# Kernel optimization log

Hardware: AMD Instinct MI355X
Metric: run time of the kernel (lower is better)

## Reference

```python
import jax, jax.numpy as jnp
import numpy as np

N = 50000      # nodes
E = 800000     # edges (before self-loops)
IN, HID, HEADS, OUT = 128, 16, 8, 64
NEG_SLOPE = 0.2
EPS = 1e-16


def gat_layer(x, edge_index, W, att_src, att_dst, bias, heads, ch, num_nodes, concat):
    # x: [N, F_in]; edge_index: [2, E'] (row0 = source j, row1 = target i)
    h = (x @ W).reshape(-1, heads, ch)                     # [N, H, C]
    a_src = jnp.sum(h * att_src, axis=-1)                  # [N, H]
    a_dst = jnp.sum(h * att_dst, axis=-1)                  # [N, H]
    src, dst = edge_index[0], edge_index[1]
    alpha = a_src[src] + a_dst[dst]                        # [E', H]
    alpha = jax.nn.leaky_relu(alpha, NEG_SLOPE)
    # segment softmax over incoming edges of each target node
    m = jax.ops.segment_max(alpha, dst, num_segments=num_nodes)
    alpha = jnp.exp(alpha - m[dst])
    denom = jax.ops.segment_sum(alpha, dst, num_segments=num_nodes)
    alpha = alpha / (denom[dst] + EPS)
    msg = h[src] * alpha[:, :, None]                       # [E', H, C]
    out = jax.ops.segment_sum(msg, dst, num_segments=num_nodes)  # [N, H, C]
    out = out.reshape(-1, heads * ch) if concat else out.mean(axis=1)
    return out + bias


def gat_model(x, edge_index, W1, att_src1, att_dst1, b1, W2, att_src2, att_dst2, b2, num_nodes):
    # PyG GATConv default add_self_loops=True
    loops = jnp.arange(num_nodes, dtype=edge_index.dtype)
    ei = jnp.concatenate([edge_index, jnp.stack([loops, loops])], axis=1)
    h = gat_layer(x, ei, W1, att_src1, att_dst1, b1, HEADS, HID, num_nodes, concat=True)
    h = jax.nn.relu(h)
    return gat_layer(h, ei, W2, att_src2, att_dst2, b2, 1, OUT, num_nodes, concat=False)


def setup_inputs() -> dict:
    key = jax.random.key(0)
    ks = jax.random.split(key, 10)
    x = jax.random.normal(ks[0], (N, IN), jnp.float32)
    edge_index = jax.random.randint(ks[1], (2, E), 0, N, dtype=jnp.int32)
    W1 = jax.random.normal(ks[2], (IN, HEADS * HID), jnp.float32) / np.sqrt(IN).astype(np.float32)
    att_src1 = jax.random.normal(ks[3], (HEADS, HID), jnp.float32) * 0.1
    att_dst1 = jax.random.normal(ks[4], (HEADS, HID), jnp.float32) * 0.1
    b1 = jnp.zeros((HEADS * HID,), jnp.float32)
    W2 = jax.random.normal(ks[5], (HEADS * HID, OUT), jnp.float32) / np.sqrt(HEADS * HID).astype(np.float32)
    att_src2 = jax.random.normal(ks[6], (1, OUT), jnp.float32) * 0.1
    att_dst2 = jax.random.normal(ks[7], (1, OUT), jnp.float32) * 0.1
    b2 = jnp.zeros((OUT,), jnp.float32)
    return {"x": x, "edge_index": edge_index, "W1": W1, "att_src1": att_src1,
            "att_dst1": att_dst1, "b1": b1, "W2": W2, "att_src2": att_src2,
            "att_dst2": att_dst2, "b2": b2, "num_nodes": N}


def reference(x, edge_index, W1, att_src1, att_dst1, b1, W2, att_src2, att_dst2, b2, num_nodes):
    return gat_model(x, edge_index, W1, att_src1, att_dst1, b1,
                     W2, att_src2, att_dst2, b2, num_nodes)
```

## Files before the change

kernel.cpp:

```cpp
#include <hip/hip_runtime.h>

#define NEG 0.2f
#define EPSV 1e-16f
#define EPB 4096
#define CAPN 64
#define CAPB (256 * 18)

typedef _Float16 h4 __attribute__((ext_vector_type(4)));
typedef _Float16 h8 __attribute__((ext_vector_type(8)));
typedef float f32x4 __attribute__((ext_vector_type(4)));

__device__ __forceinline__ float lrelu(float x) { return x > 0.f ? x : NEG * x; }

__global__ void k_setup(const float* __restrict__ W1, _Float16* __restrict__ Wt1,
                        const float* __restrict__ W2, _Float16* __restrict__ Wt2,
                        int* __restrict__ bcur, int nbuckets) {
  const int bid = blockIdx.x, tid = threadIdx.x;
  if (bid < 64) {
    int t = bid * 256 + tid;
    int c = t >> 7, k = t & 127;
    Wt1[t] = (_Float16)W1[k * 128 + c];
  } else if (bid < 96) {
    int t = (bid - 64) * 256 + tid;
    if (t < 64 * 128) {
      int c = t >> 7, k = t & 127;
      Wt2[t] = (_Float16)W2[k * 64 + c];
    }
  } else {
    if (tid < nbuckets) bcur[tid] = tid * CAPB;
  }
}

__global__ __launch_bounds__(256) void k_bin_gemm1(
    const int* __restrict__ src, const int* __restrict__ dst, int* __restrict__ bcur,
    unsigned* __restrict__ binned, int E, int nBinB, const float* __restrict__ X,
    const _Float16* __restrict__ Wt, const float* __restrict__ atts,
    const float* __restrict__ attd, _Float16* __restrict__ Hout,
    float* __restrict__ as_, float* __restrict__ ad_, int N) {
  constexpr int K = 128, XS = 136;
  __shared__ _Float16 xs[64 * XS];
  const int tid = threadIdx.x;

  if ((int)blockIdx.x < nBinB) {
    int* hist = (int*)xs;
    int* base = hist + 256;
    const int b0 = blockIdx.x * EPB;
    const int b1 = min(b0 + EPB, E);
    hist[tid] = 0;
    __syncthreads();
    for (int e = b0 + tid; e < b1; e += 256) atomicAdd(&hist[dst[e] >> 8], 1);
    __syncthreads();
    int h = hist[tid];
    if (h > 0) base[tid] = atomicAdd(&bcur[tid], h);
    __syncthreads();
    hist[tid] = 0;
    __syncthreads();
    for (int e = b0 + tid; e < b1; e += 256) {
      int d = dst[e];
      int bk = d >> 8;
      int pos = base[bk] + atomicAdd(&hist[bk], 1);
      binned[pos] = ((unsigned)(d & 255) << 16) | (unsigned)src[e];
    }
    return;
  }

  const int bid = blockIdx.x - nBinB;
  const int wv = tid >> 6, lane = tid & 63;
  const long row0 = (long)bid * 64;
  const int nrow = (int)min((long)64, (long)N - row0);

  for (int idx = tid; idx < 64 * (K / 4); idx += 256) {
    int r = idx >> 5, iw = idx & 31;
    float4 v = make_float4(0.f, 0.f, 0.f, 0.f);
    if (r < nrow) v = *(const float4*)&X[(row0 + r) * K + iw * 4];
    h4 o;
    o[0] = (_Float16)v.x;
    o[1] = (_Float16)v.y;
    o[2] = (_Float16)v.z;
    o[3] = (_Float16)v.w;
    *(h4*)&xs[r * XS + iw * 4] = o;
  }
  __syncthreads();

  const int rlo = lane & 15, khi = lane >> 4;
  h8 a[4];
#pragma unroll
  for (int kb = 0; kb < 4; kb++)
    a[kb] = *(const h8*)&xs[(wv * 16 + rlo) * XS + kb * 32 + khi * 8];
  __syncthreads();

  const int orow = wv * 16 + khi * 4;
#pragma unroll
  for (int n = 0; n < 8; n++) {
    f32x4 acc = {0.f, 0.f, 0.f, 0.f};
#pragma unroll
    for (int kb = 0; kb < 4; kb++) {
      h8 b = *(const h8*)&Wt[(n * 16 + rlo) * K + kb * 32 + khi * 8];
      acc = __builtin_amdgcn_mfma_f32_16x16x32_f16(a[kb], b, acc, 0, 0, 0);
    }
#pragma unroll
    for (int r = 0; r < 4; r++) {
      _Float16 hv = (_Float16)acc[r];
      xs[(orow + r) * XS + n * 16 + rlo] = hv;
      if (orow + r < nrow) Hout[(row0 + orow + r) * 128 + n * 16 + rlo] = hv;
    }
  }
  __syncthreads();
  for (int t = tid; t < 64 * 8; t += 256) {
    int r = t >> 3, h = t & 7;
    if (r < nrow) {
      const _Float16* hp = &xs[r * XS + h * 16];
      const float* sp = &atts[h * 16];
      const float* dp = &attd[h * 16];
      float s = 0.f, d = 0.f;
#pragma unroll
      for (int c = 0; c < 16; c++) {
        float v = (float)hp[c];
        s += v * sp[c];
        d += v * dp[c];
      }
      as_[(row0 + r) * 8 + h] = s;
      ad_[(row0 + r) * 8 + h] = d;
    }
  }
}

__global__ __launch_bounds__(256) void k_unbin(const unsigned* __restrict__ binned,
                                               const int* __restrict__ bcur,
                                               unsigned short* __restrict__ csr_src,
                                               int* __restrict__ deg, int N) {
  __shared__ int cnt[256];
  const int n0 = blockIdx.x << 8;
  const int start = blockIdx.x * CAPB;
  const int end = bcur[blockIdx.x];
  cnt[threadIdx.x] = 0;
  __syncthreads();
  for (int t = start + (int)threadIdx.x; t < end; t += 256) {
    unsigned v = binned[t];
    int dl = (int)(v >> 16);
    int pos = atomicAdd(&cnt[dl], 1);
    if (pos < CAPN) csr_src[(long)(n0 + dl) * CAPN + pos] = (unsigned short)(v & 0xFFFFu);
  }
  __syncthreads();
  int n = n0 + (int)threadIdx.x;
  if (n < N) deg[n] = min(cnt[threadIdx.x], CAPN);
}

__global__ __launch_bounds__(256) void k_n1g2(
    const int* __restrict__ deg_, const unsigned short* __restrict__ csr_src,
    const _Float16* __restrict__ Hf, const float* __restrict__ as1,
    const float* __restrict__ ad1, const float* __restrict__ b1,
    const _Float16* __restrict__ Wt2, const float* __restrict__ s2,
    const float* __restrict__ dd2, _Float16* __restrict__ H2,
    float* __restrict__ as2, float* __restrict__ ad2, int N) {
  constexpr int K = 128, XS = 136;
  __shared__ _Float16 xs[64 * XS];
  const int tid = threadIdx.x;
  const int wv = tid >> 6, lane = tid & 63;
  const long row0 = (long)blockIdx.x * 64;
  const int nrow = (int)min((long)64, (long)N - row0);
  const int sub = lane >> 4, ln = lane & 15;
  const int f0 = ln * 8, hf = ln >> 1;

  for (int t = 0; t < 16; t++) {
    const int r = wv * 16 + t;
    const long i = row0 + r;
    if (i < N) {
      const int deg = deg_[i];
      const long beg = i * CAPN;
      const float adh = ad1[i * 8 + hf];
      const float pself = __expf(lrelu(as1[i * 8 + hf] + adh));
      float acc[8] = {0.f, 0.f, 0.f, 0.f, 0.f, 0.f, 0.f, 0.f};
      float sp = 0.f;
      int e = sub;
      for (; e + 4 < deg; e += 8) {
        int j0 = (int)csr_src[beg + e], j1 = (int)csr_src[beg + e + 4];
        float p0 = __expf(lrelu(as1[j0 * 8 + hf] + adh));
        float p1 = __expf(lrelu(as1[j1 * 8 + hf] + adh));
        h8 v0 = *(const h8*)&Hf[(long)j0 * 128 + f0];
        h8 v1 = *(const h8*)&Hf[(long)j1 * 128 + f0];
        sp += p0 + p1;
#pragma unroll
        for (int c = 0; c < 8; c++) acc[c] += p0 * (float)v0[c] + p1 * (float)v1[c];
      }
      for (; e < deg; e += 4) {
        int j = (int)csr_src[beg + e];
        float p = __expf(lrelu(as1[j * 8 + hf] + adh));
        h8 v = *(const h8*)&Hf[(long)j * 128 + f0];
        sp += p;
#pragma unroll
        for (int c = 0; c < 8; c++) acc[c] += p * (float)v[c];
      }
      if (sub == 0) {
        h8 hv = *(const h8*)&Hf[i * 128 + f0];
#pragma unroll
        for (int c = 0; c < 8; c++) acc[c] += pself * (float)hv[c];
      }
      sp += __shfl_xor(sp, 16);
      sp += __shfl_xor(sp, 32);
      const float rd = 1.f / (sp + pself + EPSV);
#pragma unroll
      for (int c = 0; c < 8; c++) {
        acc[c] += __shfl_xor(acc[c], 16);
        acc[c] += __shfl_xor(acc[c], 32);
      }
      if (sub == 0) {
        h8 o;
#pragma unroll
        for (int c = 0; c < 8; c++)
          o[c] = (_Float16)fmaxf(acc[c] * rd + b1[f0 + c], 0.f);
        *(h8*)&xs[r * XS + f0] = o;
      }
    } else if (sub == 0) {
      h8 z = {};
      *(h8*)&xs[r * XS + f0] = z;
    }
  }
  __syncthreads();

  const int rlo = lane & 15, khi = lane >> 4;
  h8 a[4];
#pragma unroll
  for (int kb = 0; kb < 4; kb++)
    a[kb] = *(const h8*)&xs[(wv * 16 + rlo) * XS + kb * 32 + khi * 8];
  __syncthreads();

  const int orow = wv * 16 + khi * 4;
#pragma unroll
  for (int n = 0; n < 4; n++) {
    f32x4 acc = {0.f, 0.f, 0.f, 0.f};
#pragma unroll
    for (int kb = 0; kb < 4; kb++) {
      h8 b = *(const h8*)&Wt2[(n * 16 + rlo) * K + kb * 32 + khi * 8];
      acc = __builtin_amdgcn_mfma_f32_16x16x32_f16(a[kb], b, acc, 0, 0, 0);
    }
#pragma unroll
    for (int r = 0; r < 4; r++) {
      _Float16 hv = (_Float16)acc[r];
      xs[(orow + r) * XS + n * 16 + rlo] = hv;
      if (orow + r < nrow) H2[(row0 + orow + r) * 64 + n * 16 + rlo] = hv;
    }
  }
  __syncthreads();
  for (int t = tid; t < 64; t += 256) {
    if (t < nrow) {
      const _Float16* hp = &xs[t * XS];
      float s = 0.f, d = 0.f;
#pragma unroll
      for (int c = 0; c < 64; c++) {
        float v = (float)hp[c];
        s += v * s2[c];
        d += v * dd2[c];
      }
      as2[row0 + t] = s;
      ad2[row0 + t] = d;
    }
  }
}

__global__ __launch_bounds__(256) void k_node2(const int* __restrict__ deg_,
                                               const unsigned short* __restrict__ csr_src,
                                               const _Float16* __restrict__ Hf,
                                               const float* __restrict__ as_,
                                               const float* __restrict__ ad_,
                                               const float* __restrict__ bias,
                                               float* __restrict__ out, int N) {
  const int wid = threadIdx.x >> 6, lane = threadIdx.x & 63;
  const int i = blockIdx.x * 4 + wid;
  if (i >= N) return;
  const long beg = (long)i * CAPN;
  const int deg = deg_[i];
  const int sub = lane >> 3, ln = lane & 7;
  const int f0 = ln * 8;

  const float adi = ad_[i];
  const float pself = __expf(lrelu(as_[i] + adi));
  float acc[8] = {0.f, 0.f, 0.f, 0.f, 0.f, 0.f, 0.f, 0.f};
  float sp = 0.f;

  int e = sub;
  for (; e + 8 < deg; e += 16) {
    int j0 = (int)csr_src[beg + e], j1 = (int)csr_src[beg + e + 8];
    float p0 = __expf(lrelu(as_[j0] + adi));
    float p1 = __expf(lrelu(as_[j1] + adi));
    h8 v0 = *(const h8*)&Hf[(long)j0 * 64 + f0];
    h8 v1 = *(const h8*)&Hf[(long)j1 * 64 + f0];
    sp += p0 + p1;
#pragma unroll
    for (int c = 0; c < 8; c++) acc[c] += p0 * (float)v0[c] + p1 * (float)v1[c];
  }
  for (; e < deg; e += 8) {
    int j = (int)csr_src[beg + e];
    float p = __expf(lrelu(as_[j] + adi));
    h8 v = *(const h8*)&Hf[(long)j * 64 + f0];
    sp += p;
#pragma unroll
    for (int c = 0; c < 8; c++) acc[c] += p * (float)v[c];
  }
  if (sub == 0) {
    h8 hv = *(const h8*)&Hf[(long)i * 64 + f0];
#pragma unroll
    for (int c = 0; c < 8; c++) acc[c] += pself * (float)hv[c];
  }
  sp += __shfl_xor(sp, 8);
  sp += __shfl_xor(sp, 16);
  sp += __shfl_xor(sp, 32);
  const float rd = 1.f / (sp + pself + EPSV);
#pragma unroll
  for (int c = 0; c < 8; c++) {
    acc[c] += __shfl_xor(acc[c], 8);
    acc[c] += __shfl_xor(acc[c], 16);
    acc[c] += __shfl_xor(acc[c], 32);
  }
  if (sub == 0) {
    float4 b0 = *(const float4*)&bias[f0];
    float4 b1 = *(const float4*)&bias[f0 + 4];
    float4 o0, o1;
    o0.x = acc[0] * rd + b0.x;
    o0.y = acc[1] * rd + b0.y;
    o0.z = acc[2] * rd + b0.z;
    o0.w = acc[3] * rd + b0.w;
    o1.x = acc[4] * rd + b1.x;
    o1.y = acc[5] * rd + b1.y;
    o1.z = acc[6] * rd + b1.z;
    o1.w = acc[7] * rd + b1.w;
    *(float4*)&out[(long)i * 64 + f0] = o0;
    *(float4*)&out[(long)i * 64 + f0 + 4] = o1;
  }
}

extern "C" void kernel_launch(void* const* d_in, const int* in_sizes, int n_in,
                              void* d_out, int out_size, void* d_ws, size_t ws_size,
                              hipStream_t stream) {
  const float* x = (const float*)d_in[0];
  const int* ei = (const int*)d_in[1];
  const float* W1 = (const float*)d_in[2];
  const float* s1 = (const float*)d_in[3];
  const float* dd1 = (const float*)d_in[4];
  const float* b1 = (const float*)d_in[5];
  const float* W2 = (const float*)d_in[6];
  const float* s2 = (const float*)d_in[7];
  const float* dd2 = (const float*)d_in[8];
  const float* b2 = (const float*)d_in[9];
  const int N = in_sizes[0] / 128;
  const int E = in_sizes[1] / 2;
  const int* src = ei;
  const int* dst = ei + E;
  const int nbuckets = (N + 255) >> 8;
  const int nBinB = (E + EPB - 1) / EPB;
  const int nGemmB = (N + 63) / 64;

  char* wsp = (char*)d_ws;
  _Float16* Wt1 = (_Float16*)wsp;
  _Float16* Wt2 = Wt1 + 128 * 128;
  _Float16* Hh = Wt2 + 64 * 128;
  float* as1 = (float*)((char*)Hh + (size_t)N * 128 * sizeof(_Float16));
  float* ad1 = as1 + (size_t)N * 8;
  _Float16* H2 = (_Float16*)(ad1 + (size_t)N * 8);
  float* as2 = (float*)(H2 + (size_t)N * 64);
  float* ad2 = as2 + N;
  int* deg = (int*)(ad2 + N);
  unsigned short* csr_src = (unsigned short*)(deg + N);
  int* bcur = (int*)(csr_src + (size_t)N * CAPN);
  unsigned* binned = (unsigned*)(bcur + 256);
  float* out = (float*)d_out;

  dim3 B(256);

  k_setup<<<dim3(97), B, 0, stream>>>(W1, Wt1, W2, Wt2, bcur, nbuckets);

  k_bin_gemm1<<<dim3(nBinB + nGemmB), B, 0, stream>>>(
      src, dst, bcur, binned, E, nBinB, x, Wt1, s1, dd1, Hh, as1, ad1, N);

  k_unbin<<<dim3(nbuckets), B, 0, stream>>>(binned, bcur, csr_src, deg, N);

  k_n1g2<<<dim3(nGemmB), B, 0, stream>>>(deg, csr_src, Hh, as1, ad1, b1, Wt2, s2, dd2,
                                         H2, as2, ad2, N);

  k_node2<<<dim3((N + 3) / 4), B, 0, stream>>>(deg, csr_src, H2, as2, ad2, b2, out, N);
}
```

Measured before the change: 140.5 us.

## Split fused layer-1 aggregation and GEMM2 into separate node and GEMM kernels

```diff
diff --git a/kernel.cpp b/kernel.cpp
--- a/kernel.cpp
+++ b/kernel.cpp
@@ -146,74 +146,39 @@
   if (n < N) deg[n] = min(cnt[threadIdx.x], CAPN);
 }
 
-__global__ __launch_bounds__(256) void k_n1g2(
-    const int* __restrict__ deg_, const unsigned short* __restrict__ csr_src,
-    const _Float16* __restrict__ Hf, const float* __restrict__ as1,
-    const float* __restrict__ ad1, const float* __restrict__ b1,
-    const _Float16* __restrict__ Wt2, const float* __restrict__ s2,
-    const float* __restrict__ dd2, _Float16* __restrict__ H2,
-    float* __restrict__ as2, float* __restrict__ ad2, int N) {
+template <int M, int H, int C, typename TX>
+__global__ __launch_bounds__(256) void k_gemm_mfma(const TX* __restrict__ X,
+                                                   const _Float16* __restrict__ Wt,
+                                                   const float* __restrict__ atts,
+                                                   const float* __restrict__ attd,
+                                                   _Float16* __restrict__ Hout,
+                                                   float* __restrict__ as_,
+                                                   float* __restrict__ ad_, int N) {
   constexpr int K = 128, XS = 136;
   __shared__ _Float16 xs[64 * XS];
   const int tid = threadIdx.x;
   const int wv = tid >> 6, lane = tid & 63;
   const long row0 = (long)blockIdx.x * 64;
   const int nrow = (int)min((long)64, (long)N - row0);
-  const int sub = lane >> 4, ln = lane & 15;
-  const int f0 = ln * 8, hf = ln >> 1;
-
-  for (int t = 0; t < 16; t++) {
-    const int r = wv * 16 + t;
-    const long i = row0 + r;
-    if (i < N) {
-      const int deg = deg_[i];
-      const long beg = i * CAPN;
-      const float adh = ad1[i * 8 + hf];
-      const float pself = __expf(lrelu(as1[i * 8 + hf] + adh));
-      float acc[8] = {0.f, 0.f, 0.f, 0.f, 0.f, 0.f, 0.f, 0.f};
-      float sp = 0.f;
-      int e = sub;
-      for (; e + 4 < deg; e += 8) {
-        int j0 = (int)csr_src[beg + e], j1 = (int)csr_src[beg + e + 4];
-        float p0 = __expf(lrelu(as1[j0 * 8 + hf] + adh));
-        float p1 = __expf(lrelu(as1[j1 * 8 + hf] + adh));
-        h8 v0 = *(const h8*)&Hf[(long)j0 * 128 + f0];
-        h8 v1 = *(const h8*)&Hf[(long)j1 * 128 + f0];
-        sp += p0 + p1;
-#pragma unroll
-        for (int c = 0; c < 8; c++) acc[c] += p0 * (float)v0[c] + p1 * (float)v1[c];
-      }
-      for (; e < deg; e += 4) {
-        int j = (int)csr_src[beg + e];
-        float p = __expf(lrelu(as1[j * 8 + hf] + adh));
-        h8 v = *(const h8*)&Hf[(long)j * 128 + f0];
-        sp += p;
-#pragma unroll
-        for (int c = 0; c < 8; c++) acc[c] += p * (float)v[c];
-      }
-      if (sub == 0) {
-        h8 hv = *(const h8*)&Hf[i * 128 + f0];
-#pragma unroll
-        for (int c = 0; c < 8; c++) acc[c] += pself * (float)hv[c];
-      }
-      sp += __shfl_xor(sp, 16);
-      sp += __shfl_xor(sp, 32);
-      const float rd = 1.f / (sp + pself + EPSV);
-#pragma unroll
-      for (int c = 0; c < 8; c++) {
-        acc[c] += __shfl_xor(acc[c], 16);
-        acc[c] += __shfl_xor(acc[c], 32);
-      }
-      if (sub == 0) {
-        h8 o;
-#pragma unroll
-        for (int c = 0; c < 8; c++)
-          o[c] = (_Float16)fmaxf(acc[c] * rd + b1[f0 + c], 0.f);
-        *(h8*)&xs[r * XS + f0] = o;
-      }
-    } else if (sub == 0) {
-      h8 z = {};
-      *(h8*)&xs[r * XS + f0] = z;
+
+  if constexpr (sizeof(TX) == 4) {
+    for (int idx = tid; idx < 64 * (K / 4); idx += 256) {
+      int r = idx >> 5, iw = idx & 31;
+      float4 v = make_float4(0.f, 0.f, 0.f, 0.f);
+      if (r < nrow) v = *(const float4*)&X[(row0 + r) * K + iw * 4];
+      h4 o;
+      o[0] = (_Float16)v.x;
+      o[1] = (_Float16)v.y;
+      o[2] = (_Float16)v.z;
+      o[3] = (_Float16)v.w;
+      *(h4*)&xs[r * XS + iw * 4] = o;
+    }
+  } else {
+    for (int idx = tid; idx < 64 * (K / 8); idx += 256) {
+      int r = idx >> 4, iw = idx & 15;
+      h8 v = {};
+      if (r < nrow) v = *(const h8*)&X[(row0 + r) * K + iw * 8];
+      *(h8*)&xs[r * XS + iw * 8] = v;
     }
   }
   __syncthreads();
@@ -225,36 +190,102 @@
     a[kb] = *(const h8*)&xs[(wv * 16 + rlo) * XS + kb * 32 + khi * 8];
   __syncthreads();
 
+  constexpr int NT = M / 16;
   const int orow = wv * 16 + khi * 4;
 #pragma unroll
-  for (int n = 0; n < 4; n++) {
+  for (int n = 0; n < NT; n++) {
     f32x4 acc = {0.f, 0.f, 0.f, 0.f};
 #pragma unroll
     for (int kb = 0; kb < 4; kb++) {
-      h8 b = *(const h8*)&Wt2[(n * 16 + rlo) * K + kb * 32 + khi * 8];
+      h8 b = *(const h8*)&Wt[(n * 16 + rlo) * K + kb * 32 + khi * 8];
       acc = __builtin_amdgcn_mfma_f32_16x16x32_f16(a[kb], b, acc, 0, 0, 0);
     }
 #pragma unroll
     for (int r = 0; r < 4; r++) {
       _Float16 hv = (_Float16)acc[r];
       xs[(orow + r) * XS + n * 16 + rlo] = hv;
-      if (orow + r < nrow) H2[(row0 + orow + r) * 64 + n * 16 + rlo] = hv;
-    }
-  }
-  __syncthreads();
-  for (int t = tid; t < 64; t += 256) {
-    if (t < nrow) {
-      const _Float16* hp = &xs[t * XS];
+      if (orow + r < nrow)
+        Hout[(row0 + orow + r) * M + n * 16 + rlo] = hv;
+    }
+  }
+  __syncthreads();
+  for (int t = tid; t < 64 * H; t += 256) {
+    int r = t / H, h = t - r * H;
+    if (r < nrow) {
+      const _Float16* hp = &xs[r * XS + h * C];
+      const float* sp = &atts[h * C];
+      const float* dp = &attd[h * C];
       float s = 0.f, d = 0.f;
 #pragma unroll
-      for (int c = 0; c < 64; c++) {
+      for (int c = 0; c < C; c++) {
         float v = (float)hp[c];
-        s += v * s2[c];
-        d += v * dd2[c];
+        s += v * sp[c];
+        d += v * dp[c];
       }
-      as2[row0 + t] = s;
-      ad2[row0 + t] = d;
-    }
+      as_[(row0 + r) * H + h] = s;
+      ad_[(row0 + r) * H + h] = d;
+    }
+  }
+}
+
+__global__ __launch_bounds__(256) void k_node1(const int* __restrict__ deg_,
+                                               const unsigned short* __restrict__ csr_src,
+                                               const _Float16* __restrict__ Hf,
+                                               const float* __restrict__ as_,
+                                               const float* __restrict__ ad_,
+                                               const float* __restrict__ bias,
+                                               _Float16* __restrict__ out, int N) {
+  const int wid = threadIdx.x >> 6, lane = threadIdx.x & 63;
+  const int i = blockIdx.x * 4 + wid;
+  if (i >= N) return;
+  const long beg = (long)i * CAPN;
+  const int deg = deg_[i];
+  const int sub = lane >> 4, ln = lane & 15;
+  const int f0 = ln * 8, hf = ln >> 1;
+
+  const float adh = ad_[i * 8 + hf];
+  const float pself = __expf(lrelu(as_[i * 8 + hf] + adh));
+  float acc[8] = {0.f, 0.f, 0.f, 0.f, 0.f, 0.f, 0.f, 0.f};
+  float sp = 0.f;
+
+  int e = sub;
+  for (; e + 4 < deg; e += 8) {
+    int j0 = (int)csr_src[beg + e], j1 = (int)csr_src[beg + e + 4];
+    float p0 = __expf(lrelu(as_[j0 * 8 + hf] + adh));
+    float p1 = __expf(lrelu(as_[j1 * 8 + hf] + adh));
+    h8 v0 = *(const h8*)&Hf[(long)j0 * 128 + f0];
+    h8 v1 = *(const h8*)&Hf[(long)j1 * 128 + f0];
+    sp += p0 + p1;
+#pragma unroll
+    for (int c = 0; c < 8; c++) acc[c] += p0 * (float)v0[c] + p1 * (float)v1[c];
+  }
+  for (; e < deg; e += 4) {
+    int j = (int)csr_src[beg + e];
+    float p = __expf(lrelu(as_[j * 8 + hf] + adh));
+    h8 v = *(const h8*)&Hf[(long)j * 128 + f0];
+    sp += p;
+#pragma unroll
+    for (int c = 0; c < 8; c++) acc[c] += p * (float)v[c];
+  }
+  if (sub == 0) {
+    h8 hv = *(const h8*)&Hf[(long)i * 128 + f0];
+#pragma unroll
+    for (int c = 0; c < 8; c++) acc[c] += pself * (float)hv[c];
+  }
+  sp += __shfl_xor(sp, 16);
+  sp += __shfl_xor(sp, 32);
+  const float rd = 1.f / (sp + pself + EPSV);
+#pragma unroll
+  for (int c = 0; c < 8; c++) {
+    acc[c] += __shfl_xor(acc[c], 16);
+    acc[c] += __shfl_xor(acc[c], 32);
+  }
+  if (sub == 0) {
+    h8 o;
+#pragma unroll
+    for (int c = 0; c < 8; c++)
+      o[c] = (_Float16)fmaxf(acc[c] * rd + bias[f0 + c], 0.f);
+    *(h8*)&out[(long)i * 128 + f0] = o;
   }
 }
 
@@ -356,10 +387,8 @@
   _Float16* Hh = Wt2 + 64 * 128;
   float* as1 = (float*)((char*)Hh + (size_t)N * 128 * sizeof(_Float16));
   float* ad1 = as1 + (size_t)N * 8;
-  _Float16* H2 = (_Float16*)(ad1 + (size_t)N * 8);
-  float* as2 = (float*)(H2 + (size_t)N * 64);
-  float* ad2 = as2 + N;
-  int* deg = (int*)(ad2 + N);
+  _Float16* X2h = (_Float16*)(ad1 + (size_t)N * 8);
+  int* deg = (int*)(X2h + (size_t)N * 128);
   unsigned short* csr_src = (unsigned short*)(deg + N);
   int* bcur = (int*)(csr_src + (size_t)N * CAPN);
   unsigned* binned = (unsigned*)(bcur + 256);
@@ -374,8 +403,10 @@
 
   k_unbin<<<dim3(nbuckets), B, 0, stream>>>(binned, bcur, csr_src, deg, N);
 
-  k_n1g2<<<dim3(nGemmB), B, 0, stream>>>(deg, csr_src, Hh, as1, ad1, b1, Wt2, s2, dd2,
-                                         H2, as2, ad2, N);
-
-  k_node2<<<dim3((N + 3) / 4), B, 0, stream>>>(deg, csr_src, H2, as2, ad2, b2, out, N);
-}
+  k_node1<<<dim3((N + 3) / 4), B, 0, stream>>>(deg, csr_src, Hh, as1, ad1, b1, X2h, N);
+
+  k_gemm_mfma<64, 1, 64, _Float16><<<dim3(nGemmB), B, 0, stream>>>(
+      X2h, Wt2, s2, dd2, Hh, as1, ad1, N);
+
+  k_node2<<<dim3((N + 3) / 4), B, 0, stream>>>(deg, csr_src, Hh, as1, ad1, b2, out, N);
+}
```

Measured after the change: 126.4 us (median of 2 runs). 10.0% less time.
